# Performance work log

Measured on AMD Instinct MI355X. Metric: run time of the kernel, lower is better.

Reference implementation:

```python
import jax, jax.numpy as jnp
import numpy as np

N_NODES = 50000
N_EDGES = 800000
HIDDEN = 128
BN_EPS = 1e-5


def setup_inputs() -> dict:
    key = jax.random.key(0)
    k_h, k_e, k_wl, k_wr = jax.random.split(key, 4)
    h = jax.random.normal(k_h, (N_NODES, HIDDEN), dtype=jnp.float32)
    edge_index = jax.random.randint(k_e, (2, N_EDGES), 0, N_NODES, dtype=jnp.int32)
    W_l = jax.random.normal(k_wl, (HIDDEN, HIDDEN), dtype=jnp.float32) / np.sqrt(HIDDEN)
    b_l = jnp.zeros((HIDDEN,), dtype=jnp.float32)
    W_r = jax.random.normal(k_wr, (HIDDEN, HIDDEN), dtype=jnp.float32) / np.sqrt(HIDDEN)
    gamma = jnp.ones((HIDDEN,), dtype=jnp.float32)
    beta = jnp.zeros((HIDDEN,), dtype=jnp.float32)
    return {"h": h, "edge_index": edge_index, "W_l": W_l, "b_l": b_l,
            "W_r": W_r, "gamma": gamma, "beta": beta}


def reference(h, edge_index, W_l, b_l, W_r, gamma, beta):
    # SAGEConv(aggr='mean'): out_i = W_l @ mean_{j->i} h_j + b_l + W_r @ h_i
    src = edge_index[0]  # message sources
    dst = edge_index[1]  # message targets
    n = h.shape[0]
    msg_sum = jax.ops.segment_sum(h[src], dst, num_segments=n)          # [N, D]
    deg = jax.ops.segment_sum(jnp.ones_like(dst, dtype=h.dtype), dst, num_segments=n)
    agg = msg_sum / jnp.maximum(deg, 1.0)[:, None]                      # mean aggregation
    out = agg @ W_l.T + b_l + h @ W_r.T                                 # [N, D]
    # BatchNorm1d (training mode: batch statistics, biased variance)
    mean = jnp.mean(out, axis=0)
    var = jnp.var(out, axis=0)
    out = gamma * (out - mean) * jax.lax.rsqrt(var + BN_EPS) + beta
    out = jax.nn.relu(out)
    # dropout p=0.0 -> identity; residual add
    return out + h
```

## Files before the change

### kernel.cpp

```cpp
#include <hip/hip_runtime.h>

#define N_NODES 50000
#define N_EDGES 800000
#define HIDDEN  128
#define BN_EPS  1e-5f
#define SLOT    64

typedef __attribute__((ext_vector_type(8))) short short8;
typedef __attribute__((ext_vector_type(4))) float f32x4;

__device__ inline unsigned short f2bf(float x) {
    unsigned u = __float_as_uint(x);
    return (unsigned short)((u + 0x7FFFu + ((u >> 16) & 1u)) >> 16);
}
__device__ inline void cvt8(const float* x, short8& hi, short8& lo) {
#pragma unroll
    for (int i = 0; i < 8; i++) {
        unsigned u = __float_as_uint(x[i]);
        unsigned r = (u + 0x7FFFu + ((u >> 16) & 1u)) & 0xFFFF0000u;
        hi[i] = (short)(r >> 16);
        float res = x[i] - __uint_as_float(r);
        lo[i] = (short)f2bf(res);
    }
}

__global__ __launch_bounds__(256) void bin_kernel(
    const int* __restrict__ edge_index,
    const float* __restrict__ W_l,
    const float* __restrict__ W_r,
    int* __restrict__ cnt,
    int* __restrict__ slots,
    unsigned short* __restrict__ WhiG,
    unsigned short* __restrict__ WloG,
    float* __restrict__ bn_acc)
{
    const int gid = blockIdx.x * 256 + threadIdx.x;
    if (blockIdx.x < 128) {
        const int n = gid >> 8;
        const int k = gid & 255;
        const float w = (k < 128) ? W_l[n * 128 + k] : W_r[n * 128 + (k - 128)];
        unsigned u = __float_as_uint(w);
        unsigned r = (u + 0x7FFFu + ((u >> 16) & 1u)) & 0xFFFF0000u;
        WhiG[gid] = (unsigned short)(r >> 16);
        WloG[gid] = f2bf(w - __uint_as_float(r));
    }
    if (blockIdx.x == 128) bn_acc[threadIdx.x] = 0.0f;

    if (gid < N_EDGES) {
        const int d = edge_index[N_EDGES + gid];
        const int s = edge_index[gid];
        const int pos = atomicAdd(&cnt[d], 1);
        if (pos < SLOT) slots[(size_t)d * SLOT + pos] = s;
    }
}

__global__ __launch_bounds__(256) void gather_kernel(
    const float* __restrict__ h,
    const int* __restrict__ cnt,
    const int* __restrict__ slots,
    float* __restrict__ agg)
{
    const int WPP = N_NODES / 4;
    const int gwave = (blockIdx.x * 256 + threadIdx.x) >> 6;
    const int pass = gwave / WPP;
    const int w    = gwave - pass * WPP;
    const int group = (threadIdx.x >> 4) & 3;
    const int sub   = threadIdx.x & 15;
    const int n  = w * 4 + group;
    const int fo = pass * 64 + sub * 4;

    int c = cnt[n];
    c = (c > SLOT) ? SLOT : c;
    const int* sl = slots + (size_t)n * SLOT;

    float4 acc = make_float4(0.0f, 0.0f, 0.0f, 0.0f);
    int j = 0;
    for (; j + 4 <= c; j += 4) {
        const int s0 = sl[j], s1 = sl[j + 1], s2 = sl[j + 2], s3 = sl[j + 3];
        const float4 v0 = *reinterpret_cast<const float4*>(h + (size_t)s0 * HIDDEN + fo);
        const float4 v1 = *reinterpret_cast<const float4*>(h + (size_t)s1 * HIDDEN + fo);
        const float4 v2 = *reinterpret_cast<const float4*>(h + (size_t)s2 * HIDDEN + fo);
        const float4 v3 = *reinterpret_cast<const float4*>(h + (size_t)s3 * HIDDEN + fo);
        acc.x += (v0.x + v1.x) + (v2.x + v3.x);
        acc.y += (v0.y + v1.y) + (v2.y + v3.y);
        acc.z += (v0.z + v1.z) + (v2.z + v3.z);
        acc.w += (v0.w + v1.w) + (v2.w + v3.w);
    }
    for (; j < c; j++) {
        const float4 v0 = *reinterpret_cast<const float4*>(h + (size_t)sl[j] * HIDDEN + fo);
        acc.x += v0.x; acc.y += v0.y; acc.z += v0.z; acc.w += v0.w;
    }
    const float inv = 1.0f / (float)((c > 0) ? c : 1);
    acc.x *= inv; acc.y *= inv; acc.z *= inv; acc.w *= inv;
    *reinterpret_cast<float4*>(agg + (size_t)n * HIDDEN + fo) = acc;
}

__global__ __launch_bounds__(256) void gemm_kernel(
    const float* __restrict__ agg,
    const float* __restrict__ h,
    const unsigned short* __restrict__ WhiG,
    const unsigned short* __restrict__ WloG,
    const float* __restrict__ b_l,
    float* __restrict__ out,
    float* __restrict__ bn_acc)
{
    __shared__ short WsH[128][64];
    __shared__ short WsL[128][64];
    __shared__ float bnS[128];
    __shared__ float bnS2[128];

    const int tid  = threadIdx.x;
    const int lane = tid & 63;
    const int wv   = tid >> 6;
    const int row0 = blockIdx.x * 128;
    const int colb = lane & 15;
    const int quad = lane >> 4;

    if (tid < 128) { bnS[tid] = 0.0f; bnS2[tid] = 0.0f; }

    f32x4 acc[2][8];
#pragma unroll
    for (int s = 0; s < 2; s++)
#pragma unroll
        for (int c = 0; c < 8; c++) acc[s][c] = (f32x4)(0.0f);

    const int wcol  = tid >> 1;
    const int sbase = (tid & 1) * 4;

    for (int kc = 0; kc < 4; kc++) {
        const float* X = (kc < 2) ? agg : h;
        const int kb = (kc & 1) * 64;
        const int kw = kc * 64;

        __syncthreads();
#pragma unroll
        for (int j = 0; j < 4; j++) {
            const int slot = sbase + j;
            short8 vh = *reinterpret_cast<const short8*>(WhiG + (size_t)wcol * 256 + kw + slot * 8);
            short8 vl = *reinterpret_cast<const short8*>(WloG + (size_t)wcol * 256 + kw + slot * 8);
            const int sp = slot ^ (wcol & 7);
            *reinterpret_cast<short8*>(&WsH[wcol][sp * 8]) = vh;
            *reinterpret_cast<short8*>(&WsL[wcol][sp * 8]) = vl;
        }
        __syncthreads();

#pragma unroll
        for (int ks = 0; ks < 2; ks++) {
            short8 ahi[2], alo[2];
#pragma unroll
            for (int sub = 0; sub < 2; sub++) {
                int row = row0 + wv * 32 + sub * 16 + colb;
                row = (row < N_NODES) ? row : (N_NODES - 1);
                const float* xp = X + (size_t)row * HIDDEN + kb + ks * 32 + quad * 8;
                float xr[8];
                const float4 p0 = *reinterpret_cast<const float4*>(xp);
                const float4 p1 = *reinterpret_cast<const float4*>(xp + 4);
                xr[0] = p0.x; xr[1] = p0.y; xr[2] = p0.z; xr[3] = p0.w;
                xr[4] = p1.x; xr[5] = p1.y; xr[6] = p1.z; xr[7] = p1.w;
                cvt8(xr, ahi[sub], alo[sub]);
            }
#pragma unroll
            for (int c = 0; c < 8; c++) {
                const int bc = c * 16 + colb;
                const int sp = (ks * 4 + quad) ^ (bc & 7);
                short8 bhi = *reinterpret_cast<const short8*>(&WsH[bc][sp * 8]);
                short8 blo = *reinterpret_cast<const short8*>(&WsL[bc][sp * 8]);
#pragma unroll
                for (int sub = 0; sub < 2; sub++) {
                    acc[sub][c] = __builtin_amdgcn_mfma_f32_16x16x32_bf16(ahi[sub], bhi, acc[sub][c], 0, 0, 0);
                    acc[sub][c] = __builtin_amdgcn_mfma_f32_16x16x32_bf16(ahi[sub], blo, acc[sub][c], 0, 0, 0);
                    acc[sub][c] = __builtin_amdgcn_mfma_f32_16x16x32_bf16(alo[sub], bhi, acc[sub][c], 0, 0, 0);
                }
            }
        }
    }

#pragma unroll
    for (int c = 0; c < 8; c++) {
        const int col = c * 16 + colb;
        const float bias = b_l[col];
        float s = 0.0f, s2 = 0.0f;
#pragma unroll
        for (int sub = 0; sub < 2; sub++) {
            const int rbase = row0 + wv * 32 + sub * 16 + quad * 4;
#pragma unroll
            for (int reg = 0; reg < 4; reg++) {
                const int r = rbase + reg;
                if (r < N_NODES) {
                    const float o = acc[sub][c][reg] + bias;
                    out[(size_t)r * HIDDEN + col] = o;
                    s += o; s2 += o * o;
                }
            }
        }
        atomicAdd(&bnS[col], s);
        atomicAdd(&bnS2[col], s2);
    }
    __syncthreads();
    if (tid < 128) {
        atomicAdd(&bn_acc[tid], bnS[tid]);
        atomicAdd(&bn_acc[128 + tid], bnS2[tid]);
    }
}

__global__ __launch_bounds__(256) void bn_apply_kernel(
    const float* __restrict__ h,
    const float* __restrict__ gamma,
    const float* __restrict__ beta,
    const float* __restrict__ bn_acc,
    float* __restrict__ out)
{
    const float inv_n = 1.0f / (float)N_NODES;
    const size_t total = (size_t)N_NODES * HIDDEN;
    size_t idx = ((size_t)blockIdx.x * blockDim.x + threadIdx.x) * 4;
    const size_t stride = (size_t)gridDim.x * blockDim.x * 4;

    for (; idx < total; idx += stride) {
        const int col = (int)(idx & (HIDDEN - 1));
        float4 x  = *reinterpret_cast<float4*>(out + idx);
        float4 sm = *reinterpret_cast<const float4*>(bn_acc + col);
        float4 sq = *reinterpret_cast<const float4*>(bn_acc + HIDDEN + col);
        float4 g  = *reinterpret_cast<const float4*>(gamma + col);
        float4 bt = *reinterpret_cast<const float4*>(beta + col);
        float4 hr = *reinterpret_cast<const float4*>(h + idx);

        float4 res;
        {
            float m = sm.x * inv_n; float var = sq.x * inv_n - m * m;
            float v = g.x * (x.x - m) * rsqrtf(var + BN_EPS) + bt.x;
            res.x = fmaxf(v, 0.0f) + hr.x;
        }
        {
            float m = sm.y * inv_n; float var = sq.y * inv_n - m * m;
            float v = g.y * (x.y - m) * rsqrtf(var + BN_EPS) + bt.y;
            res.y = fmaxf(v, 0.0f) + hr.y;
        }
        {
            float m = sm.z * inv_n; float var = sq.z * inv_n - m * m;
            float v = g.z * (x.z - m) * rsqrtf(var + BN_EPS) + bt.z;
            res.z = fmaxf(v, 0.0f) + hr.z;
        }
        {
            float m = sm.w * inv_n; float var = sq.w * inv_n - m * m;
            float v = g.w * (x.w - m) * rsqrtf(var + BN_EPS) + bt.w;
            res.w = fmaxf(v, 0.0f) + hr.w;
        }
        *reinterpret_cast<float4*>(out + idx) = res;
    }
}

extern "C" void kernel_launch(void* const* d_in, const int* in_sizes, int n_in,
                              void* d_out, int out_size, void* d_ws, size_t ws_size,
                              hipStream_t stream)
{
    const float* h          = (const float*)d_in[0];
    const int*   edge_index = (const int*)d_in[1];
    const float* W_l        = (const float*)d_in[2];
    const float* b_l        = (const float*)d_in[3];
    const float* W_r        = (const float*)d_in[4];
    const float* gamma      = (const float*)d_in[5];
    const float* beta       = (const float*)d_in[6];
    float* out = (float*)d_out;

    char* ws = (char*)d_ws;
    int*   cnt   = (int*)ws;
    int*   slots = cnt + N_NODES;
    float* agg   = (float*)(slots + (size_t)N_NODES * SLOT);
    unsigned short* WhiG = (unsigned short*)(agg + (size_t)N_NODES * HIDDEN);
    unsigned short* WloG = WhiG + 128 * 256;
    float* bn_acc = (float*)(WloG + 128 * 256);

    hipMemsetAsync(cnt, 0, (size_t)N_NODES * sizeof(int), stream);

    bin_kernel<<<(N_EDGES + 255) / 256, 256, 0, stream>>>(
        edge_index, W_l, W_r, cnt, slots, WhiG, WloG, bn_acc);

    gather_kernel<<<(2 * (N_NODES / 4) + 3) / 4, 256, 0, stream>>>(h, cnt, slots, agg);

    gemm_kernel<<<(N_NODES + 127) / 128, 256, 0, stream>>>(
        agg, h, WhiG, WloG, b_l, out, bn_acc);

    bn_apply_kernel<<<2048, 256, 0, stream>>>(h, gamma, beta, bn_acc, out);
}
```

Before: 235.2 us.

## Build exact CSR via count-scan-place and gather bf16 features into bf16 aggregate

Replaces the fixed 64-slot binning with a proper CSR: count degrees, a single-block prefix scan, then a second atomic pass that places 16-bit source ids. The gather now reads a bf16 copy of h, made in the prep kernel, and writes a bf16 aggregate. The GEMM loads that aggregate directly and drops the lo-part MFMA for the aggregate half. This halves gather bandwidth and removes the slot cap, at the cost of extra kernel launches, a serial single-block scan, a second atomic pass, and reduced precision in the aggregated features.

Measured after the change: 334.2 us. +42.1%, slower.

```diff
diff --git a/kernel.cpp b/kernel.cpp
--- a/kernel.cpp
+++ b/kernel.cpp
@@ -4,14 +4,17 @@
 #define N_EDGES 800000
 #define HIDDEN  128
 #define BN_EPS  1e-5f
-#define SLOT    64
 
 typedef __attribute__((ext_vector_type(8))) short short8;
+typedef __attribute__((ext_vector_type(8))) unsigned short ushort8;
 typedef __attribute__((ext_vector_type(4))) float f32x4;
 
 __device__ inline unsigned short f2bf(float x) {
     unsigned u = __float_as_uint(x);
     return (unsigned short)((u + 0x7FFFu + ((u >> 16) & 1u)) >> 16);
+}
+__device__ inline float bf2f(unsigned short u) {
+    return __uint_as_float(((unsigned)u) << 16);
 }
 __device__ inline void cvt8(const float* x, short8& hi, short8& lo) {
 #pragma unroll
@@ -19,23 +22,41 @@
         unsigned u = __float_as_uint(x[i]);
         unsigned r = (u + 0x7FFFu + ((u >> 16) & 1u)) & 0xFFFF0000u;
         hi[i] = (short)(r >> 16);
-        float res = x[i] - __uint_as_float(r);
-        lo[i] = (short)f2bf(res);
-    }
-}
-
-__global__ __launch_bounds__(256) void bin_kernel(
+        lo[i] = (short)f2bf(x[i] - __uint_as_float(r));
+    }
+}
+
+#define NB_EDGE 3125
+#define NB_HB   3125
+#define NB_W    128
+
+__global__ __launch_bounds__(256) void prep_kernel(
     const int* __restrict__ edge_index,
+    const float* __restrict__ h,
     const float* __restrict__ W_l,
     const float* __restrict__ W_r,
     int* __restrict__ cnt,
-    int* __restrict__ slots,
+    unsigned short* __restrict__ hb,
     unsigned short* __restrict__ WhiG,
     unsigned short* __restrict__ WloG,
     float* __restrict__ bn_acc)
 {
-    const int gid = blockIdx.x * 256 + threadIdx.x;
-    if (blockIdx.x < 128) {
+    const int b = blockIdx.x;
+    const int tid = threadIdx.x;
+    if (b < NB_EDGE) {
+        const int e = b * 256 + tid;
+        atomicAdd(&cnt[edge_index[N_EDGES + e]], 1);
+    } else if (b < NB_EDGE + NB_HB) {
+        if (b == NB_EDGE) bn_acc[tid] = 0.0f;
+        const size_t i8 = ((size_t)(b - NB_EDGE) * 256 + tid) * 8;
+        const float4 p0 = *reinterpret_cast<const float4*>(h + i8);
+        const float4 p1 = *reinterpret_cast<const float4*>(h + i8 + 4);
+        ushort8 v;
+        v[0] = f2bf(p0.x); v[1] = f2bf(p0.y); v[2] = f2bf(p0.z); v[3] = f2bf(p0.w);
+        v[4] = f2bf(p1.x); v[5] = f2bf(p1.y); v[6] = f2bf(p1.z); v[7] = f2bf(p1.w);
+        *reinterpret_cast<ushort8*>(hb + i8) = v;
+    } else {
+        const int gid = (b - NB_EDGE - NB_HB) * 256 + tid;
         const int n = gid >> 8;
         const int k = gid & 255;
         const float w = (k < 128) ? W_l[n * 128 + k] : W_r[n * 128 + (k - 128)];
@@ -44,59 +65,96 @@
         WhiG[gid] = (unsigned short)(r >> 16);
         WloG[gid] = f2bf(w - __uint_as_float(r));
     }
-    if (blockIdx.x == 128) bn_acc[threadIdx.x] = 0.0f;
-
-    if (gid < N_EDGES) {
-        const int d = edge_index[N_EDGES + gid];
-        const int s = edge_index[gid];
-        const int pos = atomicAdd(&cnt[d], 1);
-        if (pos < SLOT) slots[(size_t)d * SLOT + pos] = s;
-    }
+}
+
+__global__ __launch_bounds__(1024) void scan_kernel(
+    const int* __restrict__ cnt,
+    int* __restrict__ rp)
+{
+    const int C = 49;
+    const int t = threadIdx.x;
+    const int base = t * C;
+    int s = 0;
+    for (int i = 0; i < C; i++) {
+        const int idx = base + i;
+        if (idx < N_NODES) s += cnt[idx];
+    }
+    __shared__ int ps[1024];
+    ps[t] = s;
+    __syncthreads();
+    for (int off = 1; off < 1024; off <<= 1) {
+        const int v = (t >= off) ? ps[t - off] : 0;
+        __syncthreads();
+        ps[t] += v;
+        __syncthreads();
+    }
+    int run = (t > 0) ? ps[t - 1] : 0;
+    if (t == 1023) rp[N_NODES] = run;
+    for (int i = 0; i < C; i++) {
+        const int idx = base + i;
+        if (idx < N_NODES) { rp[idx] = run; run += cnt[idx]; }
+    }
+}
+
+__global__ __launch_bounds__(256) void place_kernel(
+    const int* __restrict__ edge_index,
+    const int* __restrict__ rp,
+    int* __restrict__ cur,
+    unsigned short* __restrict__ csr)
+{
+    const int e = blockIdx.x * 256 + threadIdx.x;
+    const int d = edge_index[N_EDGES + e];
+    const int s = edge_index[e];
+    const int pos = atomicAdd(&cur[d], 1);
+    csr[rp[d] + pos] = (unsigned short)s;
 }
 
 __global__ __launch_bounds__(256) void gather_kernel(
-    const float* __restrict__ h,
-    const int* __restrict__ cnt,
-    const int* __restrict__ slots,
-    float* __restrict__ agg)
-{
-    const int WPP = N_NODES / 4;
-    const int gwave = (blockIdx.x * 256 + threadIdx.x) >> 6;
-    const int pass = gwave / WPP;
-    const int w    = gwave - pass * WPP;
+    const unsigned short* __restrict__ hb,
+    const int* __restrict__ rp,
+    const unsigned short* __restrict__ csr,
+    unsigned short* __restrict__ aggb)
+{
     const int group = (threadIdx.x >> 4) & 3;
     const int sub   = threadIdx.x & 15;
-    const int n  = w * 4 + group;
-    const int fo = pass * 64 + sub * 4;
-
-    int c = cnt[n];
-    c = (c > SLOT) ? SLOT : c;
-    const int* sl = slots + (size_t)n * SLOT;
-
-    float4 acc = make_float4(0.0f, 0.0f, 0.0f, 0.0f);
+    const int wave  = (blockIdx.x * 256 + threadIdx.x) >> 6;
+    const int n = wave * 4 + group;
+    if (n >= N_NODES) return;
+
+    const int base = rp[n];
+    const int c = rp[n + 1] - base;
+    const int fo = sub * 8;
+
+    float acc[8];
+#pragma unroll
+    for (int i = 0; i < 8; i++) acc[i] = 0.0f;
+
     int j = 0;
     for (; j + 4 <= c; j += 4) {
-        const int s0 = sl[j], s1 = sl[j + 1], s2 = sl[j + 2], s3 = sl[j + 3];
-        const float4 v0 = *reinterpret_cast<const float4*>(h + (size_t)s0 * HIDDEN + fo);
-        const float4 v1 = *reinterpret_cast<const float4*>(h + (size_t)s1 * HIDDEN + fo);
-        const float4 v2 = *reinterpret_cast<const float4*>(h + (size_t)s2 * HIDDEN + fo);
-        const float4 v3 = *reinterpret_cast<const float4*>(h + (size_t)s3 * HIDDEN + fo);
-        acc.x += (v0.x + v1.x) + (v2.x + v3.x);
-        acc.y += (v0.y + v1.y) + (v2.y + v3.y);
-        acc.z += (v0.z + v1.z) + (v2.z + v3.z);
-        acc.w += (v0.w + v1.w) + (v2.w + v3.w);
+        const int s0 = csr[base + j],     s1 = csr[base + j + 1];
+        const int s2 = csr[base + j + 2], s3 = csr[base + j + 3];
+        const ushort8 v0 = *reinterpret_cast<const ushort8*>(hb + (size_t)s0 * HIDDEN + fo);
+        const ushort8 v1 = *reinterpret_cast<const ushort8*>(hb + (size_t)s1 * HIDDEN + fo);
+        const ushort8 v2 = *reinterpret_cast<const ushort8*>(hb + (size_t)s2 * HIDDEN + fo);
+        const ushort8 v3 = *reinterpret_cast<const ushort8*>(hb + (size_t)s3 * HIDDEN + fo);
+#pragma unroll
+        for (int i = 0; i < 8; i++)
+            acc[i] += (bf2f(v0[i]) + bf2f(v1[i])) + (bf2f(v2[i]) + bf2f(v3[i]));
     }
     for (; j < c; j++) {
-        const float4 v0 = *reinterpret_cast<const float4*>(h + (size_t)sl[j] * HIDDEN + fo);
-        acc.x += v0.x; acc.y += v0.y; acc.z += v0.z; acc.w += v0.w;
+        const ushort8 v0 = *reinterpret_cast<const ushort8*>(hb + (size_t)csr[base + j] * HIDDEN + fo);
+#pragma unroll
+        for (int i = 0; i < 8; i++) acc[i] += bf2f(v0[i]);
     }
     const float inv = 1.0f / (float)((c > 0) ? c : 1);
-    acc.x *= inv; acc.y *= inv; acc.z *= inv; acc.w *= inv;
-    *reinterpret_cast<float4*>(agg + (size_t)n * HIDDEN + fo) = acc;
+    ushort8 o;
+#pragma unroll
+    for (int i = 0; i < 8; i++) o[i] = f2bf(acc[i] * inv);
+    *reinterpret_cast<ushort8*>(aggb + (size_t)n * HIDDEN + fo) = o;
 }
 
 __global__ __launch_bounds__(256) void gemm_kernel(
-    const float* __restrict__ agg,
+    const unsigned short* __restrict__ aggb,
     const float* __restrict__ h,
     const unsigned short* __restrict__ WhiG,
     const unsigned short* __restrict__ WloG,
@@ -128,7 +186,6 @@
     const int sbase = (tid & 1) * 4;
 
     for (int kc = 0; kc < 4; kc++) {
-        const float* X = (kc < 2) ? agg : h;
         const int kb = (kc & 1) * 64;
         const int kw = kc * 64;
 
@@ -151,13 +208,18 @@
             for (int sub = 0; sub < 2; sub++) {
                 int row = row0 + wv * 32 + sub * 16 + colb;
                 row = (row < N_NODES) ? row : (N_NODES - 1);
-                const float* xp = X + (size_t)row * HIDDEN + kb + ks * 32 + quad * 8;
-                float xr[8];
-                const float4 p0 = *reinterpret_cast<const float4*>(xp);
-                const float4 p1 = *reinterpret_cast<const float4*>(xp + 4);
-                xr[0] = p0.x; xr[1] = p0.y; xr[2] = p0.z; xr[3] = p0.w;
-                xr[4] = p1.x; xr[5] = p1.y; xr[6] = p1.z; xr[7] = p1.w;
-                cvt8(xr, ahi[sub], alo[sub]);
+                if (kc < 2) {
+                    ahi[sub] = *reinterpret_cast<const short8*>(
+                        aggb + (size_t)row * HIDDEN + kb + ks * 32 + quad * 8);
+                } else {
+                    const float* xp = h + (size_t)row * HIDDEN + kb + ks * 32 + quad * 8;
+                    float xr[8];
+                    const float4 p0 = *reinterpret_cast<const float4*>(xp);
+                    const float4 p1 = *reinterpret_cast<const float4*>(xp + 4);
+                    xr[0] = p0.x; xr[1] = p0.y; xr[2] = p0.z; xr[3] = p0.w;
+                    xr[4] = p1.x; xr[5] = p1.y; xr[6] = p1.z; xr[7] = p1.w;
+                    cvt8(xr, ahi[sub], alo[sub]);
+                }
             }
 #pragma unroll
             for (int c = 0; c < 8; c++) {
@@ -169,7 +231,8 @@
                 for (int sub = 0; sub < 2; sub++) {
                     acc[sub][c] = __builtin_amdgcn_mfma_f32_16x16x32_bf16(ahi[sub], bhi, acc[sub][c], 0, 0, 0);
                     acc[sub][c] = __builtin_amdgcn_mfma_f32_16x16x32_bf16(ahi[sub], blo, acc[sub][c], 0, 0, 0);
-                    acc[sub][c] = __builtin_amdgcn_mfma_f32_16x16x32_bf16(alo[sub], bhi, acc[sub][c], 0, 0, 0);
+                    if (kc >= 2)
+                        acc[sub][c] = __builtin_amdgcn_mfma_f32_16x16x32_bf16(alo[sub], bhi, acc[sub][c], 0, 0, 0);
                 }
             }
         }
@@ -263,22 +326,30 @@
     float* out = (float*)d_out;
 
     char* ws = (char*)d_ws;
-    int*   cnt   = (int*)ws;
-    int*   slots = cnt + N_NODES;
-    float* agg   = (float*)(slots + (size_t)N_NODES * SLOT);
-    unsigned short* WhiG = (unsigned short*)(agg + (size_t)N_NODES * HIDDEN);
-    unsigned short* WloG = WhiG + 128 * 256;
-    float* bn_acc = (float*)(WloG + 128 * 256);
-
-    hipMemsetAsync(cnt, 0, (size_t)N_NODES * sizeof(int), stream);
-
-    bin_kernel<<<(N_EDGES + 255) / 256, 256, 0, stream>>>(
-        edge_index, W_l, W_r, cnt, slots, WhiG, WloG, bn_acc);
-
-    gather_kernel<<<(2 * (N_NODES / 4) + 3) / 4, 256, 0, stream>>>(h, cnt, slots, agg);
+    int* cnt = (int*)ws;
+    int* rp  = cnt + 50000;
+    unsigned short* csr  = (unsigned short*)(rp + 50004);
+    unsigned short* hb   = csr + 800000;
+    unsigned short* aggb = hb + 6400000;
+    unsigned short* WhiG = aggb + 6400000;
+    unsigned short* WloG = WhiG + 32768;
+    float* bn_acc = (float*)(WloG + 32768);
+
+    hipMemsetAsync(cnt, 0, 50000 * sizeof(int), stream);
+
+    prep_kernel<<<NB_EDGE + NB_HB + NB_W, 256, 0, stream>>>(
+        edge_index, h, W_l, W_r, cnt, hb, WhiG, WloG, bn_acc);
+
+    scan_kernel<<<1, 1024, 0, stream>>>(cnt, rp);
+
+    hipMemsetAsync(cnt, 0, 50000 * sizeof(int), stream);
+
+    place_kernel<<<NB_EDGE, 256, 0, stream>>>(edge_index, rp, cnt, csr);
+
+    gather_kernel<<<(N_NODES / 4 + 3) / 4, 256, 0, stream>>>(hb, rp, csr, aggb);
 
     gemm_kernel<<<(N_NODES + 127) / 128, 256, 0, stream>>>(
-        agg, h, WhiG, WloG, b_l, out, bn_acc);
+        aggb, h, WhiG, WloG, b_l, out, bn_acc);
 
     bn_apply_kernel<<<2048, 256, 0, stream>>>(h, gamma, beta, bn_acc, out);
 }
```
